# Kernel optimization log

Hardware: AMD Instinct MI355X
Metric: run time of the kernel (lower is better)

Reference implementation:

```python
import jax, jax.numpy as jnp
import numpy as np

BITS = 4
MAXQ = (1 << BITS) - 1  # 15
PACK_BITS = 32
GROUP_SIZE = 128


def setup_inputs() -> dict:
    key = jax.random.key(0)
    k1, k2, k3, k4, k5 = jax.random.split(key, 5)
    in_f, out_f, tokens = 4096, 11008, 8192
    pack_factor = PACK_BITS // BITS  # 8
    n_groups = in_f // GROUP_SIZE  # 32
    x = jax.random.normal(k1, (tokens, in_f), dtype=jnp.float32)
    qweight = jax.random.randint(k2, (in_f // pack_factor, out_f), 0, 2147483647, dtype=jnp.int32)
    qzeros = jax.random.randint(k3, (n_groups, out_f // pack_factor), 0, 2147483647, dtype=jnp.int32)
    scales = jax.random.uniform(k4, (n_groups, out_f), dtype=jnp.float32) * 0.01 + 1e-3
    bias = jax.random.normal(k5, (out_f,), dtype=jnp.float32)
    g_idx = (jnp.arange(in_f, dtype=jnp.int32) // GROUP_SIZE).astype(jnp.int32)
    return {"x": x, "qweight": qweight, "qzeros": qzeros, "scales": scales, "bias": bias, "g_idx": g_idx}


def _dequantize(qweight, qzeros, scales, g_idx, in_features):
    # wf = [0, 4, 8, ..., 28]
    shifts = jnp.arange(0, PACK_BITS, BITS, dtype=jnp.int32)
    # unpack zeros: [G, out/8] -> [G, out/8, 8] -> [G, out]
    zeros = (qzeros[:, :, None] >> shifts[None, None, :]) & MAXQ
    zeros = zeros.reshape(scales.shape)
    # unpack weight: [in/8, out] -> [in/8, 8, out] -> [in, out]
    w = (qweight[:, None, :] >> shifts[None, :, None]) & MAXQ
    w = w.reshape(-1, scales.shape[1])[:in_features]
    # dequant: scales[g_idx] * (w - zeros[g_idx])
    return scales[g_idx] * (w - zeros[g_idx]).astype(scales.dtype)


def reference(x, qweight, qzeros, scales, bias, g_idx):
    W = _dequantize(qweight, qzeros, scales, g_idx, x.shape[1])  # [in, out]
    return x @ W + bias
```

## Files before the change

### kernel.cpp

```cpp
#include <hip/hip_runtime.h>
#include <hip/hip_bf16.h>

typedef __attribute__((ext_vector_type(8))) short short8;
typedef __attribute__((ext_vector_type(4))) float f32x4;
typedef __attribute__((ext_vector_type(4))) unsigned int uint4v;

#define BM 128
#define BN 128
#define BK 64

__device__ __forceinline__ void gl_lds16(const __hip_bfloat16* g, __hip_bfloat16* l) {
  __builtin_amdgcn_global_load_lds((const __attribute__((address_space(1))) void*)g,
                                   (__attribute__((address_space(3))) void*)l,
                                   16, 0, 0);
}

__global__ void dequant_kernel(const int* __restrict__ qweight,
                               const int* __restrict__ qzeros,
                               const float* __restrict__ scales,
                               __hip_bfloat16* __restrict__ wp, int N, int K) {
  const int n = blockIdx.x * 256 + threadIdx.x;
  const int kc = blockIdx.y;
  const int g = kc >> 4;
  const float s = scales[(size_t)g * N + n];
  const int zq = qzeros[(size_t)g * (N >> 3) + (n >> 3)];
  const float c = s * (float)((zq >> ((n & 7) * 4)) & 15);
  const int q = qweight[(size_t)kc * N + n];
  __hip_bfloat16 v[8];
#pragma unroll
  for (int j = 0; j < 8; j++)
    v[j] = __float2bfloat16(fmaf(s, (float)((q >> (4 * j)) & 15), -c));
  ((uint4v*)wp)[(size_t)kc * N + n] = *(const uint4v*)v;
}

__global__ void cvtx_kernel(const float* __restrict__ x,
                            __hip_bfloat16* __restrict__ xp, int M, int K) {
  __shared__ __hip_bfloat16 tile[64 * 64];
  const int t = threadIdx.x;
  const int m0 = blockIdx.x * 64, k0 = blockIdx.y * 64;
  const int mr = t >> 2, cq = t & 3;
  const float4* src = (const float4*)(x + (size_t)(m0 + mr) * K + k0 + cq * 16);
  const float4 a = src[0], b = src[1], c = src[2], d = src[3];
  __hip_bfloat16 v[16];
  v[0] = __float2bfloat16(a.x);  v[1] = __float2bfloat16(a.y);
  v[2] = __float2bfloat16(a.z);  v[3] = __float2bfloat16(a.w);
  v[4] = __float2bfloat16(b.x);  v[5] = __float2bfloat16(b.y);
  v[6] = __float2bfloat16(b.z);  v[7] = __float2bfloat16(b.w);
  v[8] = __float2bfloat16(c.x);  v[9] = __float2bfloat16(c.y);
  v[10] = __float2bfloat16(c.z); v[11] = __float2bfloat16(c.w);
  v[12] = __float2bfloat16(d.x); v[13] = __float2bfloat16(d.y);
  v[14] = __float2bfloat16(d.z); v[15] = __float2bfloat16(d.w);
  *(uint4v*)&tile[((cq * 2 + 0) * 64 + mr) * 8] = *(const uint4v*)&v[0];
  *(uint4v*)&tile[((cq * 2 + 1) * 64 + mr) * 8] = *(const uint4v*)&v[8];
  __syncthreads();
#pragma unroll
  for (int j = 0; j < 2; j++) {
    const int s = j * 256 + t;
    const int c8 = s >> 6, m = s & 63;
    ((uint4v*)xp)[(size_t)((k0 >> 3) + c8) * M + m0 + m] = *(const uint4v*)&tile[s * 8];
  }
}

__global__ __launch_bounds__(256) void gemm_kernel(
    const __hip_bfloat16* __restrict__ Xp,
    const __hip_bfloat16* __restrict__ Wp,
    const float* __restrict__ bias,
    float* __restrict__ C, int M, int N, int K) {
  __shared__ __hip_bfloat16 As[BM * BK];
  __shared__ __hip_bfloat16 Bs[BN * BK];
  const int tid = threadIdx.x;
  const int m0 = blockIdx.x * BM;
  const int n0 = blockIdx.y * BN;
  const int wv = tid >> 6, ln = tid & 63;
  const int wm = (wv & 1) * 64, wn = (wv >> 1) * 64;
  const int lr = ln & 15, q4 = ln >> 4;

  f32x4 acc[4][4] = {};

  const int K8 = K >> 3;
  for (int kt8 = 0; kt8 < K8; kt8 += 8) {
#pragma unroll
    for (int i = 0; i < 4; i++) {
      const int s = i * 256 + tid;
      const int c8 = s >> 7, ml = s & 127;
      gl_lds16(Xp + ((size_t)(kt8 + c8) * M + m0 + ml) * 8, &As[s * 8]);
    }
#pragma unroll
    for (int i = 0; i < 4; i++) {
      const int s = i * 256 + tid;
      const int c8 = s >> 7, nl = s & 127;
      gl_lds16(Wp + ((size_t)(kt8 + c8) * N + n0 + nl) * 8, &Bs[s * 8]);
    }
    __syncthreads();
#pragma unroll
    for (int ks = 0; ks < 2; ks++) {
      const int q = ks * 4 + q4;
      short8 af[4], bf[4];
#pragma unroll
      for (int mf = 0; mf < 4; mf++)
        af[mf] = *(const short8*)&As[q * 1024 + (wm + mf * 16 + lr) * 8];
#pragma unroll
      for (int nf = 0; nf < 4; nf++)
        bf[nf] = *(const short8*)&Bs[q * 1024 + (wn + nf * 16 + lr) * 8];
#pragma unroll
      for (int mf = 0; mf < 4; mf++)
#pragma unroll
        for (int nf = 0; nf < 4; nf++)
          acc[mf][nf] = __builtin_amdgcn_mfma_f32_16x16x32_bf16(
              af[mf], bf[nf], acc[mf][nf], 0, 0, 0);
    }
    __syncthreads();
  }

  const int cr = m0 + wm + q4 * 4;
  const int cc = n0 + wn + lr;
#pragma unroll
  for (int nf = 0; nf < 4; nf++) {
    const float bv = bias[cc + nf * 16];
#pragma unroll
    for (int mf = 0; mf < 4; mf++) {
#pragma unroll
      for (int r = 0; r < 4; r++) {
        C[(size_t)(cr + mf * 16 + r) * N + cc + nf * 16] = acc[mf][nf][r] + bv;
      }
    }
  }
}

__global__ void naive_kernel(const float* __restrict__ x, const int* __restrict__ qweight,
                             const int* __restrict__ qzeros, const float* __restrict__ scales,
                             const float* __restrict__ bias, const int* __restrict__ g_idx,
                             float* __restrict__ out, int in_f, int out_f) {
  const int n = blockIdx.x * blockDim.x + threadIdx.x;
  if (n >= out_f) return;
  const int m = blockIdx.y;
  const float* xr = x + (size_t)m * in_f;
  float acc = 0.f;
  for (int kk = 0; kk < (in_f >> 3); kk++) {
    const int q = qweight[(size_t)kk * out_f + n];
    const int g = g_idx[kk * 8];
    const float s = scales[(size_t)g * out_f + n];
    const int z = (qzeros[(size_t)g * (out_f >> 3) + (n >> 3)] >> ((n & 7) * 4)) & 15;
    float part = 0.f;
#pragma unroll
    for (int j = 0; j < 8; j++)
      part += xr[kk * 8 + j] * (float)(((q >> (4 * j)) & 15) - z);
    acc += s * part;
  }
  out[(size_t)m * out_f + n] = acc + bias[n];
}

extern "C" void kernel_launch(void* const* d_in, const int* in_sizes, int n_in,
                              void* d_out, int out_size, void* d_ws, size_t ws_size,
                              hipStream_t stream) {
  const float* x = (const float*)d_in[0];
  const int* qweight = (const int*)d_in[1];
  const int* qzeros = (const int*)d_in[2];
  const float* scales = (const float*)d_in[3];
  const float* bias = (const float*)d_in[4];
  const int* g_idx = (const int*)d_in[5];
  float* out = (float*)d_out;

  const int out_f = in_sizes[4];
  const int in_f = in_sizes[5];
  const int tokens = in_sizes[0] / in_f;

  const size_t need_w = (size_t)in_f * out_f * sizeof(__hip_bfloat16);
  const size_t need_x = (size_t)tokens * in_f * sizeof(__hip_bfloat16);

  if (ws_size >= need_w + need_x && (in_f % 128) == 0 && (out_f % 256) == 0 &&
      (tokens % BM) == 0) {
    __hip_bfloat16* wp = (__hip_bfloat16*)d_ws;
    __hip_bfloat16* xp = (__hip_bfloat16*)((char*)d_ws + need_w);
    dequant_kernel<<<dim3(out_f / 256, in_f / 8), 256, 0, stream>>>(
        qweight, qzeros, scales, wp, out_f, in_f);
    cvtx_kernel<<<dim3(tokens / 64, in_f / 64), 256, 0, stream>>>(x, xp, tokens, in_f);
    gemm_kernel<<<dim3(tokens / BM, out_f / BN), 256, 0, stream>>>(
        xp, wp, bias, out, tokens, out_f, in_f);
  } else {
    naive_kernel<<<dim3((out_f + 255) / 256, tokens), 256, 0, stream>>>(
        x, qweight, qzeros, scales, bias, g_idx, out, in_f, out_f);
  }
}
```

Measured before the change: 1.433 ms.

## Use 256x256 double-buffered GEMM tiles with 8 waves and interleaved prefetch

Grows the GEMM block tile from 128x128 to 256x256 and runs it with 512 threads (8 waves), each wave computing a 128x64 sub-tile. It double-buffers the A and B tiles in LDS and issues the next tiles' global-to-LDS loads in pieces between four MFMA phases, using explicit vmcnt/lgkmcnt waits, barriers and s_setprio. The goal is to hide global load latency and raise data reuse per LDS byte. In exchange it uses about 128KB of LDS, so only one block fits per CU. The grid of 256x256 tiles also gives a coarser tail across the CUs.

```diff
diff --git a/kernel.cpp b/kernel.cpp
--- a/kernel.cpp
+++ b/kernel.cpp
@@ -5,8 +5,8 @@
 typedef __attribute__((ext_vector_type(4))) float f32x4;
 typedef __attribute__((ext_vector_type(4))) unsigned int uint4v;
 
-#define BM 128
-#define BN 128
+#define BM 256
+#define BN 256
 #define BK 64
 
 __device__ __forceinline__ void gl_lds16(const __hip_bfloat16* g, __hip_bfloat16* l) {
@@ -61,66 +61,139 @@
   }
 }
 
-__global__ __launch_bounds__(256) void gemm_kernel(
+__global__ __launch_bounds__(512, 2) void gemm_kernel(
     const __hip_bfloat16* __restrict__ Xp,
     const __hip_bfloat16* __restrict__ Wp,
     const float* __restrict__ bias,
     float* __restrict__ C, int M, int N, int K) {
-  __shared__ __hip_bfloat16 As[BM * BK];
-  __shared__ __hip_bfloat16 Bs[BN * BK];
+  __shared__ __hip_bfloat16 As[2][8 * 256 * 8];
+  __shared__ __hip_bfloat16 Bs[2][8 * 256 * 8];
   const int tid = threadIdx.x;
   const int m0 = blockIdx.x * BM;
   const int n0 = blockIdx.y * BN;
-  const int wv = tid >> 6, ln = tid & 63;
-  const int wm = (wv & 1) * 64, wn = (wv >> 1) * 64;
+  const int wid = tid >> 6, ln = tid & 63;
+  const int wmoff = (wid >> 2) * 128;
+  const int wnoff = (wid & 3) * 64;
   const int lr = ln & 15, q4 = ln >> 4;
 
-  f32x4 acc[4][4] = {};
-
-  const int K8 = K >> 3;
-  for (int kt8 = 0; kt8 < K8; kt8 += 8) {
-#pragma unroll
-    for (int i = 0; i < 4; i++) {
-      const int s = i * 256 + tid;
-      const int c8 = s >> 7, ml = s & 127;
-      gl_lds16(Xp + ((size_t)(kt8 + c8) * M + m0 + ml) * 8, &As[s * 8]);
-    }
-#pragma unroll
-    for (int i = 0; i < 4; i++) {
-      const int s = i * 256 + tid;
-      const int c8 = s >> 7, nl = s & 127;
-      gl_lds16(Wp + ((size_t)(kt8 + c8) * N + n0 + nl) * 8, &Bs[s * 8]);
-    }
-    __syncthreads();
-#pragma unroll
-    for (int ks = 0; ks < 2; ks++) {
-      const int q = ks * 4 + q4;
-      short8 af[4], bf[4];
-#pragma unroll
-      for (int mf = 0; mf < 4; mf++)
-        af[mf] = *(const short8*)&As[q * 1024 + (wm + mf * 16 + lr) * 8];
-#pragma unroll
-      for (int nf = 0; nf < 4; nf++)
-        bf[nf] = *(const short8*)&Bs[q * 1024 + (wn + nf * 16 + lr) * 8];
-#pragma unroll
-      for (int mf = 0; mf < 4; mf++)
-#pragma unroll
-        for (int nf = 0; nf < 4; nf++)
-          acc[mf][nf] = __builtin_amdgcn_mfma_f32_16x16x32_bf16(
-              af[mf], bf[nf], acc[mf][nf], 0, 0, 0);
-    }
-    __syncthreads();
-  }
-
-  const int cr = m0 + wm + q4 * 4;
-  const int cc = n0 + wn + lr;
-#pragma unroll
-  for (int nf = 0; nf < 4; nf++) {
+  f32x4 acc[8][4] = {};
+  const int NT = K >> 6;
+
+  auto stageA = [&](int t, int hs, int buf) {
+#pragma unroll
+    for (int i = 0; i < 2; ++i) {
+      const int s = i * 512 + tid;
+      const int c8 = (hs << 2) + (s >> 8);
+      const int row = s & 255;
+      gl_lds16(Xp + ((size_t)(t * 8 + c8) * M + m0 + row) * 8,
+               &As[buf][(c8 * 256 + row) * 8]);
+    }
+  };
+  auto stageB = [&](int t, int hs, int buf) {
+#pragma unroll
+    for (int i = 0; i < 2; ++i) {
+      const int s = i * 512 + tid;
+      const int c8 = (hs << 2) + (s >> 8);
+      const int row = s & 255;
+      gl_lds16(Wp + ((size_t)(t * 8 + c8) * N + n0 + row) * 8,
+               &Bs[buf][(c8 * 256 + row) * 8]);
+    }
+  };
+
+  stageA(0, 0, 0); stageA(0, 1, 0); stageB(0, 0, 0); stageB(0, 1, 0);
+  if (NT > 1) {
+    stageA(1, 0, 1); stageB(1, 0, 1); stageA(1, 1, 1);
+    asm volatile("s_waitcnt vmcnt(6)" ::: "memory");
+  } else {
+    asm volatile("s_waitcnt vmcnt(0)" ::: "memory");
+  }
+  __builtin_amdgcn_s_barrier();
+
+  short8 af[8], bf[2];
+
+  for (int t = 0; t < NT; ++t) {
+    const int cur = t & 1, nxt = cur ^ 1;
+    const __hip_bfloat16* Ac = As[cur];
+    const __hip_bfloat16* Bc = Bs[cur];
+
+#pragma unroll
+    for (int mf = 0; mf < 8; ++mf)
+      af[mf] = *(const short8*)&Ac[(q4 * 256 + wmoff + mf * 16 + lr) * 8];
+#pragma unroll
+    for (int j = 0; j < 2; ++j)
+      bf[j] = *(const short8*)&Bc[(q4 * 256 + wnoff + j * 16 + lr) * 8];
+    if (t + 1 < NT) stageB(t + 1, 1, nxt);
+    __builtin_amdgcn_s_barrier();
+    asm volatile("s_waitcnt lgkmcnt(0)" ::: "memory");
+    __builtin_amdgcn_s_setprio(1);
+#pragma unroll
+    for (int mf = 0; mf < 8; ++mf) {
+      acc[mf][0] = __builtin_amdgcn_mfma_f32_16x16x32_bf16(af[mf], bf[0], acc[mf][0], 0, 0, 0);
+      acc[mf][1] = __builtin_amdgcn_mfma_f32_16x16x32_bf16(af[mf], bf[1], acc[mf][1], 0, 0, 0);
+    }
+    __builtin_amdgcn_s_setprio(0);
+    __builtin_amdgcn_s_barrier();
+
+#pragma unroll
+    for (int j = 0; j < 2; ++j)
+      bf[j] = *(const short8*)&Bc[(q4 * 256 + wnoff + (2 + j) * 16 + lr) * 8];
+    if (t + 2 < NT) stageA(t + 2, 0, cur);
+    __builtin_amdgcn_s_barrier();
+    asm volatile("s_waitcnt lgkmcnt(0)" ::: "memory");
+    __builtin_amdgcn_s_setprio(1);
+#pragma unroll
+    for (int mf = 0; mf < 8; ++mf) {
+      acc[mf][2] = __builtin_amdgcn_mfma_f32_16x16x32_bf16(af[mf], bf[0], acc[mf][2], 0, 0, 0);
+      acc[mf][3] = __builtin_amdgcn_mfma_f32_16x16x32_bf16(af[mf], bf[1], acc[mf][3], 0, 0, 0);
+    }
+    __builtin_amdgcn_s_setprio(0);
+    __builtin_amdgcn_s_barrier();
+
+#pragma unroll
+    for (int mf = 0; mf < 8; ++mf)
+      af[mf] = *(const short8*)&Ac[((4 + q4) * 256 + wmoff + mf * 16 + lr) * 8];
+#pragma unroll
+    for (int j = 0; j < 2; ++j)
+      bf[j] = *(const short8*)&Bc[((4 + q4) * 256 + wnoff + j * 16 + lr) * 8];
+    if (t + 2 < NT) stageB(t + 2, 0, cur);
+    __builtin_amdgcn_s_barrier();
+    asm volatile("s_waitcnt lgkmcnt(0)" ::: "memory");
+    __builtin_amdgcn_s_setprio(1);
+#pragma unroll
+    for (int mf = 0; mf < 8; ++mf) {
+      acc[mf][0] = __builtin_amdgcn_mfma_f32_16x16x32_bf16(af[mf], bf[0], acc[mf][0], 0, 0, 0);
+      acc[mf][1] = __builtin_amdgcn_mfma_f32_16x16x32_bf16(af[mf], bf[1], acc[mf][1], 0, 0, 0);
+    }
+    __builtin_amdgcn_s_setprio(0);
+    __builtin_amdgcn_s_barrier();
+
+#pragma unroll
+    for (int j = 0; j < 2; ++j)
+      bf[j] = *(const short8*)&Bc[((4 + q4) * 256 + wnoff + (2 + j) * 16 + lr) * 8];
+    if (t + 2 < NT) stageA(t + 2, 1, cur);
+    if (t == NT - 2) asm volatile("s_waitcnt vmcnt(0)" ::: "memory");
+    else             asm volatile("s_waitcnt vmcnt(6)" ::: "memory");
+    __builtin_amdgcn_s_barrier();
+    asm volatile("s_waitcnt lgkmcnt(0)" ::: "memory");
+    __builtin_amdgcn_s_setprio(1);
+#pragma unroll
+    for (int mf = 0; mf < 8; ++mf) {
+      acc[mf][2] = __builtin_amdgcn_mfma_f32_16x16x32_bf16(af[mf], bf[0], acc[mf][2], 0, 0, 0);
+      acc[mf][3] = __builtin_amdgcn_mfma_f32_16x16x32_bf16(af[mf], bf[1], acc[mf][3], 0, 0, 0);
+    }
+    __builtin_amdgcn_s_setprio(0);
+    __builtin_amdgcn_s_barrier();
+  }
+
+  const int cr = m0 + wmoff + q4 * 4;
+  const int cc = n0 + wnoff + lr;
+#pragma unroll
+  for (int nf = 0; nf < 4; ++nf) {
     const float bv = bias[cc + nf * 16];
 #pragma unroll
-    for (int mf = 0; mf < 4; mf++) {
-#pragma unroll
-      for (int r = 0; r < 4; r++) {
+    for (int mf = 0; mf < 8; ++mf) {
+#pragma unroll
+      for (int r = 0; r < 4; ++r) {
         C[(size_t)(cr + mf * 16 + r) * N + cc + nf * 16] = acc[mf][nf][r] + bv;
       }
     }
@@ -169,13 +242,13 @@
   const size_t need_x = (size_t)tokens * in_f * sizeof(__hip_bfloat16);
 
   if (ws_size >= need_w + need_x && (in_f % 128) == 0 && (out_f % 256) == 0 &&
-      (tokens % BM) == 0) {
+      (tokens % 256) == 0) {
     __hip_bfloat16* wp = (__hip_bfloat16*)d_ws;
     __hip_bfloat16* xp = (__hip_bfloat16*)((char*)d_ws + need_w);
     dequant_kernel<<<dim3(out_f / 256, in_f / 8), 256, 0, stream>>>(
         qweight, qzeros, scales, wp, out_f, in_f);
     cvtx_kernel<<<dim3(tokens / 64, in_f / 64), 256, 0, stream>>>(x, xp, tokens, in_f);
-    gemm_kernel<<<dim3(tokens / BM, out_f / BN), 256, 0, stream>>>(
+    gemm_kernel<<<dim3(tokens / BM, out_f / BN), 512, 0, stream>>>(
         xp, wp, bias, out, tokens, out_f, in_f);
   } else {
     naive_kernel<<<dim3((out_f + 255) / 256, tokens), 256, 0, stream>>>(
```

Measured after the change: 1.198 ms. -16.4%, faster.
